# Kernel optimization log

Measured on AMD Instinct MI355X. Metric: run time of the kernel, lower is better.

Reference implementation:

```python
import jax
jax.config.update("jax_enable_x64", True)
import jax.numpy as jnp
import numpy as np

INPUT_DIM = 2048
NUM_BINS = 32
RMS_EPS = 1e-4  # RunningMeanStd initial count


def setup_inputs() -> dict:
    key = jax.random.key(0)
    k1, k2 = jax.random.split(key)
    features = jax.random.normal(k1, (64, 256, INPUT_DIM), dtype=jnp.float32)
    # register_buffer: randn(input_dim, num_bins) / sqrt(input_dim)
    random_projection = jax.random.normal(k2, (INPUT_DIM, NUM_BINS), dtype=jnp.float32) / np.sqrt(INPUT_DIM)
    return {"features": features, "random_projection": random_projection}


def _occurrence_counts(keys):
    """For each element, 1 + number of earlier elements with the same key.
    Stable argsort keeps original order inside each duplicate run, so the
    rank within a run equals the sequential visit count."""
    n = keys.shape[0]
    order = jnp.argsort(keys)  # stable
    sk = keys[order]
    idx = jnp.arange(n, dtype=jnp.int64)
    new_run = jnp.concatenate([jnp.ones((1,), bool), sk[1:] != sk[:-1]])
    starts = jax.lax.cummax(jnp.where(new_run, idx, 0))
    counts_sorted = idx - starts + 1
    return jnp.zeros(n, jnp.int64).at[order].set(counts_sorted)


def reference(features, random_projection):
    batch, seq, feat = features.shape
    x = features.reshape(-1, feat)
    n = x.shape[0]

    # RunningMeanStd.update from fresh state (mean=0, var=1, count=1e-4)
    bm = jnp.mean(x, axis=0)
    bv = jnp.var(x, axis=0, ddof=1)  # torch .var(dim=0) is unbiased
    tot = RMS_EPS + n
    mean = bm * (n / tot)  # delta = bm - 0
    m2 = 1.0 * RMS_EPS + bv * n + (bm ** 2) * (RMS_EPS * n / tot)
    var = m2 / tot
    sigma = jnp.sqrt(var + 1e-8)

    normalized = (x - mean) / sigma
    projected = normalized @ random_projection  # [n, num_bins]
    bits = (projected > 0).astype(jnp.int64)
    powers = (2 ** jnp.arange(min(NUM_BINS, 63), dtype=jnp.int64))
    h = (bits[:, : powers.shape[0]] * powers).sum(axis=-1)  # < 2^32

    env = jnp.arange(n, dtype=jnp.int64) % batch  # default env_indices path
    keys = h * batch + env  # unique per (env, hash), fits int64
    counts = _occurrence_counts(keys)

    rewards = 1.0 / jnp.sqrt(counts.astype(features.dtype))
    return rewards.reshape(batch, seq, 1)
```

## Files before the change

kernel.cpp:

```cpp
#include <hip/hip_runtime.h>
#include <math.h>

#define FEAT 2048
#define NBINS 32
#define NROWS 16384
#define NCLS 64
#define SB 1024
#define RPB 16

typedef __attribute__((ext_vector_type(8))) short short8;
typedef __attribute__((ext_vector_type(4))) float f32x4;

static __device__ __forceinline__ unsigned int pk2bf(float a, float b) {
    unsigned ua = __float_as_uint(a);
    unsigned ub = __float_as_uint(b);
    ua = (ua + 0x7FFFu + ((ua >> 16) & 1u)) >> 16;
    ub = (ub + 0x7FFFu + ((ub >> 16) & 1u)) & 0xFFFF0000u;
    return ua | ub;
}

__global__ __launch_bounds__(256) void k1_stats(const float* __restrict__ x,
                                                float* __restrict__ pS1,
                                                float* __restrict__ pS2) {
    const int b = blockIdx.x, t = threadIdx.x;
    const float4* xb = reinterpret_cast<const float4*>(x) + (size_t)b * RPB * (FEAT / 4);
    float4 s1a = make_float4(0.f,0.f,0.f,0.f), s1b = make_float4(0.f,0.f,0.f,0.f);
    float4 s2a = make_float4(0.f,0.f,0.f,0.f), s2b = make_float4(0.f,0.f,0.f,0.f);
    #pragma unroll
    for (int r = 0; r < RPB; ++r) {
        const float4 va = xb[(size_t)r * (FEAT / 4) + t];
        const float4 vb = xb[(size_t)r * (FEAT / 4) + t + 256];
        s1a.x += va.x; s1a.y += va.y; s1a.z += va.z; s1a.w += va.w;
        s2a.x += va.x * va.x; s2a.y += va.y * va.y; s2a.z += va.z * va.z; s2a.w += va.w * va.w;
        s1b.x += vb.x; s1b.y += vb.y; s1b.z += vb.z; s1b.w += vb.w;
        s2b.x += vb.x * vb.x; s2b.y += vb.y * vb.y; s2b.z += vb.z * vb.z; s2b.w += vb.w * vb.w;
    }
    float4* o1 = reinterpret_cast<float4*>(pS1 + (size_t)b * FEAT);
    float4* o2 = reinterpret_cast<float4*>(pS2 + (size_t)b * FEAT);
    o1[t] = s1a; o1[t + 256] = s1b;
    o2[t] = s2a; o2[t + 256] = s2b;
}

__global__ __launch_bounds__(256) void k2_stats(const float* __restrict__ pS1,
                                                const float* __restrict__ pS2,
                                                float* __restrict__ ms,
                                                float* __restrict__ isig_g) {
    __shared__ double sh1[32][8];
    __shared__ double sh2[32][8];
    const int t = threadIdx.x;
    const int ci = t & 7, s = t >> 3;
    const int c = blockIdx.x * 8 + ci;
    double S1 = 0.0, S2 = 0.0;
    #pragma unroll 4
    for (int j = 0; j < 32; ++j) {
        const int k = s * 32 + j;
        S1 += (double)pS1[(size_t)k * FEAT + c];
        S2 += (double)pS2[(size_t)k * FEAT + c];
    }
    sh1[s][ci] = S1; sh2[s][ci] = S2;
    __syncthreads();
    if (t < 8) {
        double s1 = 0.0, s2 = 0.0;
        #pragma unroll
        for (int q = 0; q < 32; ++q) { s1 += sh1[q][t]; s2 += sh2[q][t]; }
        const int cc = blockIdx.x * 8 + t;
        const double n = (double)NROWS;
        const double bm = s1 / n;
        const double bv = (s2 - s1 * s1 / n) / (n - 1.0);
        const double tot = 1e-4 + n;
        const double mean = bm * (n / tot);
        const double m2 = 1e-4 + bv * n + bm * bm * (1e-4 * n / tot);
        const double var = m2 / tot;
        const double isig = 1.0 / sqrt(var + 1e-8);
        ms[cc] = (float)(mean * isig);
        isig_g[cc] = (float)isig;
    }
}

__global__ __launch_bounds__(256) void k2q_frag(const float* __restrict__ isig_g,
                                                const float* __restrict__ P,
                                                unsigned int* __restrict__ QTf) {
    __shared__ float isig_sh[32];
    const int t = threadIdx.x;
    if (t < 32) isig_sh[t] = isig_g[blockIdx.x * 32 + t];
    __syncthreads();
    const int nb = t >> 7;
    const int lane = (t & 127) >> 1;
    const int half = t & 1;
    const int lrow = lane & 15, lk = lane >> 4;
    const int bin = nb * 16 + lrow;
    const int ccl = lk * 8 + half * 4;
    const int cc = blockIdx.x * 32 + ccl;
    unsigned int w0 = pk2bf(P[(size_t)cc * NBINS + bin] * isig_sh[ccl],
                            P[(size_t)(cc + 1) * NBINS + bin] * isig_sh[ccl + 1]);
    unsigned int w1 = pk2bf(P[(size_t)(cc + 2) * NBINS + bin] * isig_sh[ccl + 2],
                            P[(size_t)(cc + 3) * NBINS + bin] * isig_sh[ccl + 3]);
    const int ch = blockIdx.x >> 2, ks = blockIdx.x & 3;
    char* dst = reinterpret_cast<char*>(QTf) +
                (size_t)(((nb * 16 + ch) * 4 + ks) * 1024 + lane * 16 + half * 8);
    uint2 pk; pk.x = w0; pk.y = w1;
    *reinterpret_cast<uint2*>(dst) = pk;
}

__global__ __launch_bounds__(256) void k2b_offset(const float* __restrict__ ms,
                                                  const float* __restrict__ P,
                                                  float* __restrict__ offs) {
    __shared__ double sh[256];
    const int b = blockIdx.x, t = threadIdx.x;
    double s = 0.0;
    for (int f = t; f < FEAT; f += 256) s += (double)ms[f] * (double)P[(size_t)f * NBINS + b];
    sh[t] = s;
    __syncthreads();
    for (int st = 128; st > 0; st >>= 1) {
        if (t < st) sh[t] += sh[t + st];
        __syncthreads();
    }
    if (t == 0) offs[b] = (float)sh[0];
}

__global__ __launch_bounds__(512) void k3_mfma(const float* __restrict__ x,
                                               const unsigned int* __restrict__ QTf,
                                               const float* __restrict__ offs,
                                               unsigned int* __restrict__ hout) {
    __shared__ f32x4 red[4][2][64];
    const int t = threadIdx.x;
    const int w = t >> 6, l = t & 63;
    const int rw = w & 3, kh = w >> 2;
    const int lrow = l & 15, lk = l >> 4;
    const int bid = blockIdx.x;

    const float* ax = x + (size_t)(bid * 64 + rw * 16 + lrow) * FEAT + kh * 1024 + lk * 8;
    const short8* b0p = reinterpret_cast<const short8*>(QTf) + l + kh * 2048;
    const short8* b1p = b0p + 4096;

    f32x4 acc0 = {0.f, 0.f, 0.f, 0.f};
    f32x4 acc1 = {0.f, 0.f, 0.f, 0.f};

    #pragma unroll 8
    for (int ss = 0; ss < 32; ++ss) {
        const float4 va = *reinterpret_cast<const float4*>(ax + ss * 32);
        const float4 vb = *reinterpret_cast<const float4*>(ax + ss * 32 + 4);
        uint4 ap;
        ap.x = pk2bf(va.x, va.y); ap.y = pk2bf(va.z, va.w);
        ap.z = pk2bf(vb.x, vb.y); ap.w = pk2bf(vb.z, vb.w);
        const short8 a  = __builtin_bit_cast(short8, ap);
        const short8 b0 = b0p[ss * 64];
        const short8 b1 = b1p[ss * 64];
        acc0 = __builtin_amdgcn_mfma_f32_16x16x32_bf16(a, b0, acc0, 0, 0, 0);
        acc1 = __builtin_amdgcn_mfma_f32_16x16x32_bf16(a, b1, acc1, 0, 0, 0);
    }

    if (kh) { red[rw][0][l] = acc0; red[rw][1][l] = acc1; }
    __syncthreads();
    if (!kh) {
        const f32x4 r0 = red[rw][0][l];
        const f32x4 r1 = red[rw][1][l];
        acc0 += r0;
        acc1 += r1;
        const float o0 = offs[lrow];
        const float o1 = offs[16 + lrow];
        #pragma unroll
        for (int r = 0; r < 4; ++r) {
            const unsigned long long m0 = __ballot(acc0[r] > o0);
            const unsigned long long m1 = __ballot(acc1[r] > o1);
            if (lrow == 0) {
                const unsigned int h =
                    (unsigned int)((m0 >> (16 * lk)) & 0xFFFFull) |
                    ((unsigned int)((m1 >> (16 * lk)) & 0xFFFFull) << 16);
                const int irow = rw * 16 + lk * 4 + r;
                hout[(size_t)irow * 256 + bid] = h;
            }
        }
    }
}

__global__ __launch_bounds__(256) void k4_count(const unsigned int* __restrict__ hcls,
                                                float* __restrict__ out) {
    __shared__ unsigned int hh[256];
    const int c = blockIdx.x, t = threadIdx.x;
    hh[t] = hcls[(size_t)c * 256 + t];
    __syncthreads();
    const unsigned int mine = hh[t];
    int cnt = 1;
    for (int j = 0; j < 256; ++j) {
        cnt += (j < t && hh[j] == mine) ? 1 : 0;
    }
    out[(size_t)t * NCLS + c] = 1.0f / sqrtf((float)cnt);
}

extern "C" void kernel_launch(void* const* d_in, const int* in_sizes, int n_in,
                              void* d_out, int out_size, void* d_ws, size_t ws_size,
                              hipStream_t stream) {
    const float* x = (const float*)d_in[0];
    const float* P = (const float*)d_in[1];
    float* out = (float*)d_out;
    char* ws = (char*)d_ws;

    float* pS1 = (float*)(ws);
    float* pS2 = (float*)(ws + (size_t)SB * FEAT * 4);
    float* ms  = (float*)(ws + (size_t)16 * 1024 * 1024);
    float* isig = ms + FEAT;
    float* offsB = isig + FEAT;
    unsigned int* QTf = (unsigned int*)(ws + (size_t)17 * 1024 * 1024);
    unsigned int* h   = (unsigned int*)(ws + (size_t)18 * 1024 * 1024);

    k1_stats<<<SB, 256, 0, stream>>>(x, pS1, pS2);
    k2_stats<<<256, 256, 0, stream>>>(pS1, pS2, ms, isig);
    k2q_frag<<<64, 256, 0, stream>>>(isig, P, QTf);
    k2b_offset<<<32, 256, 0, stream>>>(ms, P, offsB);
    k3_mfma<<<256, 512, 0, stream>>>(x, QTf, offsB, h);
    k4_count<<<NCLS, 256, 0, stream>>>(h, out);
}
```

Before: 78.20 us.

## Merge prep kernels and software-pipeline MFMA projection with register prefetch

Folds the bf16 projection-fragment kernel and the offset-dot kernel into one launch, using block index to pick the role, which removes one kernel launch. The MFMA kernel drops the split-K across two wave groups and its LDS reduction. Each wave now runs the full K loop with an 8-deep register prefetch of x and projection fragments, which should hide global load latency. This raises register pressure and halves threads per block (launch_bounds 256,1), so there may be less latency hiding from occupancy.

```diff
diff --git a/kernel.cpp b/kernel.cpp
--- a/kernel.cpp
+++ b/kernel.cpp
@@ -77,99 +77,116 @@
     }
 }
 
-__global__ __launch_bounds__(256) void k2q_frag(const float* __restrict__ isig_g,
-                                                const float* __restrict__ P,
-                                                unsigned int* __restrict__ QTf) {
-    __shared__ float isig_sh[32];
+__global__ __launch_bounds__(256) void k2_misc(const float* __restrict__ isig_g,
+                                               const float* __restrict__ ms,
+                                               const float* __restrict__ P,
+                                               unsigned int* __restrict__ QTf,
+                                               float* __restrict__ offs) {
     const int t = threadIdx.x;
-    if (t < 32) isig_sh[t] = isig_g[blockIdx.x * 32 + t];
-    __syncthreads();
-    const int nb = t >> 7;
-    const int lane = (t & 127) >> 1;
-    const int half = t & 1;
-    const int lrow = lane & 15, lk = lane >> 4;
-    const int bin = nb * 16 + lrow;
-    const int ccl = lk * 8 + half * 4;
-    const int cc = blockIdx.x * 32 + ccl;
-    unsigned int w0 = pk2bf(P[(size_t)cc * NBINS + bin] * isig_sh[ccl],
-                            P[(size_t)(cc + 1) * NBINS + bin] * isig_sh[ccl + 1]);
-    unsigned int w1 = pk2bf(P[(size_t)(cc + 2) * NBINS + bin] * isig_sh[ccl + 2],
-                            P[(size_t)(cc + 3) * NBINS + bin] * isig_sh[ccl + 3]);
-    const int ch = blockIdx.x >> 2, ks = blockIdx.x & 3;
-    char* dst = reinterpret_cast<char*>(QTf) +
-                (size_t)(((nb * 16 + ch) * 4 + ks) * 1024 + lane * 16 + half * 8);
-    uint2 pk; pk.x = w0; pk.y = w1;
-    *reinterpret_cast<uint2*>(dst) = pk;
-}
-
-__global__ __launch_bounds__(256) void k2b_offset(const float* __restrict__ ms,
-                                                  const float* __restrict__ P,
-                                                  float* __restrict__ offs) {
-    __shared__ double sh[256];
-    const int b = blockIdx.x, t = threadIdx.x;
-    double s = 0.0;
-    for (int f = t; f < FEAT; f += 256) s += (double)ms[f] * (double)P[(size_t)f * NBINS + b];
-    sh[t] = s;
-    __syncthreads();
-    for (int st = 128; st > 0; st >>= 1) {
-        if (t < st) sh[t] += sh[t + st];
+    if (blockIdx.x < 64) {
+        __shared__ float isig_sh[32];
+        if (t < 32) isig_sh[t] = isig_g[blockIdx.x * 32 + t];
         __syncthreads();
-    }
-    if (t == 0) offs[b] = (float)sh[0];
-}
-
-__global__ __launch_bounds__(512) void k3_mfma(const float* __restrict__ x,
-                                               const unsigned int* __restrict__ QTf,
-                                               const float* __restrict__ offs,
-                                               unsigned int* __restrict__ hout) {
-    __shared__ f32x4 red[4][2][64];
+        const int nb = t >> 7;
+        const int lane = (t & 127) >> 1;
+        const int half = t & 1;
+        const int lrow = lane & 15, lk = lane >> 4;
+        const int bin = nb * 16 + lrow;
+        const int ccl = lk * 8 + half * 4;
+        const int cc = blockIdx.x * 32 + ccl;
+        unsigned int w0 = pk2bf(P[(size_t)cc * NBINS + bin] * isig_sh[ccl],
+                                P[(size_t)(cc + 1) * NBINS + bin] * isig_sh[ccl + 1]);
+        unsigned int w1 = pk2bf(P[(size_t)(cc + 2) * NBINS + bin] * isig_sh[ccl + 2],
+                                P[(size_t)(cc + 3) * NBINS + bin] * isig_sh[ccl + 3]);
+        const int ch = blockIdx.x >> 2, ks = blockIdx.x & 3;
+        char* dst = reinterpret_cast<char*>(QTf) +
+                    (size_t)(((nb * 16 + ch) * 4 + ks) * 1024 + lane * 16 + half * 8);
+        uint2 pk; pk.x = w0; pk.y = w1;
+        *reinterpret_cast<uint2*>(dst) = pk;
+    } else {
+        __shared__ double sh[256];
+        const int b = blockIdx.x - 64;
+        double s = 0.0;
+        for (int f = t; f < FEAT; f += 256) s += (double)ms[f] * (double)P[(size_t)f * NBINS + b];
+        sh[t] = s;
+        __syncthreads();
+        for (int st = 128; st > 0; st >>= 1) {
+            if (t < st) sh[t] += sh[t + st];
+            __syncthreads();
+        }
+        if (t == 0) offs[b] = (float)sh[0];
+    }
+}
+
+__global__ __launch_bounds__(256, 1) void k3_mfma(const float* __restrict__ x,
+                                                  const unsigned int* __restrict__ QTf,
+                                                  const float* __restrict__ offs,
+                                                  unsigned int* __restrict__ hout) {
     const int t = threadIdx.x;
     const int w = t >> 6, l = t & 63;
-    const int rw = w & 3, kh = w >> 2;
     const int lrow = l & 15, lk = l >> 4;
     const int bid = blockIdx.x;
 
-    const float* ax = x + (size_t)(bid * 64 + rw * 16 + lrow) * FEAT + kh * 1024 + lk * 8;
-    const short8* b0p = reinterpret_cast<const short8*>(QTf) + l + kh * 2048;
+    const float* ax = x + (size_t)(bid * 64 + w * 16 + lrow) * FEAT + lk * 8;
+    const short8* b0p = reinterpret_cast<const short8*>(QTf) + l;
     const short8* b1p = b0p + 4096;
 
     f32x4 acc0 = {0.f, 0.f, 0.f, 0.f};
     f32x4 acc1 = {0.f, 0.f, 0.f, 0.f};
 
-    #pragma unroll 8
-    for (int ss = 0; ss < 32; ++ss) {
-        const float4 va = *reinterpret_cast<const float4*>(ax + ss * 32);
-        const float4 vb = *reinterpret_cast<const float4*>(ax + ss * 32 + 4);
+    float4 va[8], vb[8];
+    short8 b0s[8], b1s[8];
+
+    #pragma unroll
+    for (int p = 0; p < 8; ++p) {
+        va[p] = *reinterpret_cast<const float4*>(ax + p * 32);
+        vb[p] = *reinterpret_cast<const float4*>(ax + p * 32 + 4);
+        b0s[p] = b0p[p * 64];
+        b1s[p] = b1p[p * 64];
+    }
+
+    const float* axg = ax;
+    const short8* b0g = b0p;
+    const short8* b1g = b1p;
+    #pragma unroll 1
+    for (int g = 0; g < 7; ++g) {
+        #pragma unroll
+        for (int s2 = 0; s2 < 8; ++s2) {
+            uint4 ap;
+            ap.x = pk2bf(va[s2].x, va[s2].y); ap.y = pk2bf(va[s2].z, va[s2].w);
+            ap.z = pk2bf(vb[s2].x, vb[s2].y); ap.w = pk2bf(vb[s2].z, vb[s2].w);
+            const short8 a = __builtin_bit_cast(short8, ap);
+            acc0 = __builtin_amdgcn_mfma_f32_16x16x32_bf16(a, b0s[s2], acc0, 0, 0, 0);
+            acc1 = __builtin_amdgcn_mfma_f32_16x16x32_bf16(a, b1s[s2], acc1, 0, 0, 0);
+            va[s2] = *reinterpret_cast<const float4*>(axg + (8 + s2) * 32);
+            vb[s2] = *reinterpret_cast<const float4*>(axg + (8 + s2) * 32 + 4);
+            b0s[s2] = b0g[(8 + s2) * 64];
+            b1s[s2] = b1g[(8 + s2) * 64];
+        }
+        axg += 256; b0g += 512; b1g += 512;
+    }
+    #pragma unroll
+    for (int s2 = 0; s2 < 8; ++s2) {
         uint4 ap;
-        ap.x = pk2bf(va.x, va.y); ap.y = pk2bf(va.z, va.w);
-        ap.z = pk2bf(vb.x, vb.y); ap.w = pk2bf(vb.z, vb.w);
-        const short8 a  = __builtin_bit_cast(short8, ap);
-        const short8 b0 = b0p[ss * 64];
-        const short8 b1 = b1p[ss * 64];
-        acc0 = __builtin_amdgcn_mfma_f32_16x16x32_bf16(a, b0, acc0, 0, 0, 0);
-        acc1 = __builtin_amdgcn_mfma_f32_16x16x32_bf16(a, b1, acc1, 0, 0, 0);
-    }
-
-    if (kh) { red[rw][0][l] = acc0; red[rw][1][l] = acc1; }
-    __syncthreads();
-    if (!kh) {
-        const f32x4 r0 = red[rw][0][l];
-        const f32x4 r1 = red[rw][1][l];
-        acc0 += r0;
-        acc1 += r1;
-        const float o0 = offs[lrow];
-        const float o1 = offs[16 + lrow];
-        #pragma unroll
-        for (int r = 0; r < 4; ++r) {
-            const unsigned long long m0 = __ballot(acc0[r] > o0);
-            const unsigned long long m1 = __ballot(acc1[r] > o1);
-            if (lrow == 0) {
-                const unsigned int h =
-                    (unsigned int)((m0 >> (16 * lk)) & 0xFFFFull) |
-                    ((unsigned int)((m1 >> (16 * lk)) & 0xFFFFull) << 16);
-                const int irow = rw * 16 + lk * 4 + r;
-                hout[(size_t)irow * 256 + bid] = h;
-            }
+        ap.x = pk2bf(va[s2].x, va[s2].y); ap.y = pk2bf(va[s2].z, va[s2].w);
+        ap.z = pk2bf(vb[s2].x, vb[s2].y); ap.w = pk2bf(vb[s2].z, vb[s2].w);
+        const short8 a = __builtin_bit_cast(short8, ap);
+        acc0 = __builtin_amdgcn_mfma_f32_16x16x32_bf16(a, b0s[s2], acc0, 0, 0, 0);
+        acc1 = __builtin_amdgcn_mfma_f32_16x16x32_bf16(a, b1s[s2], acc1, 0, 0, 0);
+    }
+
+    const float o0 = offs[lrow];
+    const float o1 = offs[16 + lrow];
+    #pragma unroll
+    for (int r = 0; r < 4; ++r) {
+        const unsigned long long m0 = __ballot(acc0[r] > o0);
+        const unsigned long long m1 = __ballot(acc1[r] > o1);
+        if (lrow == 0) {
+            const unsigned int h =
+                (unsigned int)((m0 >> (16 * lk)) & 0xFFFFull) |
+                ((unsigned int)((m1 >> (16 * lk)) & 0xFFFFull) << 16);
+            const int irow = w * 16 + lk * 4 + r;
+            hout[(size_t)irow * 256 + bid] = h;
         }
     }
 }
@@ -206,8 +223,7 @@
 
     k1_stats<<<SB, 256, 0, stream>>>(x, pS1, pS2);
     k2_stats<<<256, 256, 0, stream>>>(pS1, pS2, ms, isig);
-    k2q_frag<<<64, 256, 0, stream>>>(isig, P, QTf);
-    k2b_offset<<<32, 256, 0, stream>>>(ms, P, offsB);
-    k3_mfma<<<256, 512, 0, stream>>>(x, QTf, offsB, h);
+    k2_misc<<<96, 256, 0, stream>>>(isig, ms, P, QTf, offsB);
+    k3_mfma<<<256, 256, 0, stream>>>(x, QTf, offsB, h);
     k4_count<<<NCLS, 256, 0, stream>>>(h, out);
 }
```

After: 70.40 us. -10.0%, faster.
